# Optimization experiments

Measured on AMD Instinct MI355X. Metric: run time of the kernel, lower is better.

The kernel has to match this reference:

```python
import jax, jax.numpy as jnp
import numpy as np

ALPHA, GAMMA = 0.25, 2.0
THR = 0.85            # soft_target_threshold
KL_EPS = 1e-6
FOCAL_EPS = 1e-8
VOC = 96              # len(vocab); index VOC is blank/pad


def setup_inputs() -> dict:
    key = jax.random.key(0)
    ks = jax.random.split(key, 6)
    bs, nq, n_pts, num_gt, L = 16, 200, 25, 32, 25
    return {
        "pred_logits": jax.random.normal(ks[0], (bs, nq, n_pts, 1), jnp.float32),
        "pred_ctrl_points": jax.random.uniform(ks[1], (bs, nq, n_pts, 2), jnp.float32),
        "pred_text_logits": jax.random.normal(ks[2], (bs, nq, n_pts, VOC + 1), jnp.float32),
        "tgt_ctrl_points": jax.random.uniform(ks[3], (bs, num_gt, n_pts, 2), jnp.float32),
        "tgt_texts": jax.random.randint(ks[4], (bs, num_gt, L), 0, VOC + 1),
        "centroids": jax.random.normal(ks[5], (VOC, 256), jnp.float32),
    }


def _cost_matrix(pred_logits, pred_ctrl_points, pred_text_logits,
                 tgt_ctrl_points, tgt_texts, centroids):
    bs, nq, n_pts, _ = pred_logits.shape
    num_gt = tgt_texts.shape[1]

    # ---- focal classification cost (mean over control points) ----
    out_prob = jax.nn.sigmoid(pred_logits.reshape(bs * nq, n_pts, -1))
    neg = (1.0 - ALPHA) * out_prob ** GAMMA * (-jnp.log1p(-(out_prob - FOCAL_EPS)))
    neg = (1.0 - ALPHA) * out_prob ** GAMMA * (-jnp.log(1.0 - out_prob + FOCAL_EPS))
    pos = ALPHA * (1.0 - out_prob) ** GAMMA * (-jnp.log(out_prob + FOCAL_EPS))
    cost_class = (pos[..., 0] - neg[..., 0]).mean(-1, keepdims=True)  # [bs*nq, 1]

    # ---- L1 cdist over flattened control points ----
    out_pts = pred_ctrl_points.reshape(bs * nq, n_pts * 2)
    tgt_pts = tgt_ctrl_points.reshape(bs * num_gt, n_pts * 2)
    cost_kpts = jnp.abs(out_pts[:, None, :] - tgt_pts[None, :, :]).sum(-1)  # [bs*nq, bs*num_gt]

    # ---- linguistic KL-div cost (per-batch block diagonal) ----
    probs = jax.nn.softmax(pred_text_logits, axis=-1)          # [bs,nq,n_pts,VOC+1]
    pred_avg = probs[..., :VOC].mean(axis=2)                   # [bs,nq,VOC]
    P = pred_avg + KL_EPS
    P = P / P.sum(-1, keepdims=True)
    logP = jnp.log(P)

    # soft target distribution per character (generate_soft_target_sequence)
    cn = centroids / jnp.linalg.norm(centroids, axis=-1, keepdims=True)
    soft_all = THR * jnp.eye(VOC, dtype=P.dtype) + (1.0 - THR) * jax.nn.softmax(cn @ cn.T, axis=-1)  # [VOC,VOC]

    mask = (tgt_texts != VOC)                                  # [bs,num_gt,L]
    lengths = mask.sum(-1)                                     # [bs,num_gt]
    per_char = soft_all[jnp.clip(tgt_texts, 0, VOC - 1)]       # [bs,num_gt,L,VOC]
    tgt_avg = (per_char * mask[..., None]).sum(2) / jnp.maximum(lengths, 1)[..., None].astype(P.dtype)
    T = tgt_avg + KL_EPS
    T = T / T.sum(-1, keepdims=True)                           # [bs,num_gt,VOC]

    # KL(T || P) = sum T*logT - sum T*logP, vectorized over (query, gt)
    kl = (T * jnp.log(T)).sum(-1)[:, None, :] - jnp.einsum('bqv,bgv->bqg', logP, T)  # [bs,nq,num_gt]
    kl = jnp.where(lengths[:, None, :] == 0, 100.0, kl)

    # place per-batch blocks on the diagonal of the global cost matrix
    eye = jnp.eye(bs, dtype=kl.dtype)
    cost_text = jnp.einsum('bqg,bc->bqcg', kl, eye).reshape(bs * nq, bs * num_gt)

    C = 1.0 * cost_class + 1.0 * cost_kpts + 1.0 * cost_text   # class/coord/text weights = 1
    return C.reshape(bs, nq, bs * num_gt)


def reference(pred_logits, pred_ctrl_points, pred_text_logits,
              tgt_ctrl_points, tgt_texts, centroids):
    return _cost_matrix(pred_logits, pred_ctrl_points, pred_text_logits,
                        tgt_ctrl_points, tgt_texts, centroids)
```

## Files before the change

kernel.cpp:

```cpp
#include <hip/hip_runtime.h>
#include <hip/hip_bf16.h>

#define BS 16
#define NQ 200
#define NPTS 25
#define VOC 96
#define VOCP1 97
#define NGT 32
#define LSEQ 25
#define NCOL (BS*NGT)
#define NBQ (BS*NQ)
#define KL_EPS 1e-6f
#define FOCAL_EPS 1e-8f

__global__ __launch_bounds__(128) void kA(
        const float* __restrict__ pred_logits,
        const float* __restrict__ pred_text_logits,
        const float* __restrict__ centroids,
        float* __restrict__ logP,
        float* __restrict__ cost_class,
        float* __restrict__ soft)
{
    const int tid  = threadIdx.x;
    const int wave = tid >> 6, lane = tid & 63;
    __shared__ float s_buf[NPTS * VOCP1];
    __shared__ float s_invden[NPTS];
    __shared__ float s_part[2];

    if (blockIdx.x < NBQ) {
        const int bq = blockIdx.x;
        const float* tl = pred_text_logits + (size_t)bq * NPTS * VOCP1;
        for (int i = tid; i < NPTS * VOCP1; i += 128)
            s_buf[i] = __expf(tl[i]);
        __syncthreads();

        const int grp = tid >> 5, sub = tid & 31;
        for (int p0 = 0; p0 < NPTS; p0 += 4) {
            int p = p0 + grp;
            float s = 0.f;
            if (p < NPTS)
                for (int v = sub; v < VOCP1; v += 32) s += s_buf[p * VOCP1 + v];
            #pragma unroll
            for (int off = 16; off; off >>= 1) s += __shfl_xor(s, off, 32);
            if (p < NPTS && sub == 0) s_invden[p] = 1.0f / s;
        }

        if (wave == 0) {
            float cc = 0.f;
            if (lane < NPTS) {
                float x = pred_logits[bq * NPTS + lane];
                float p = 1.f / (1.f + __expf(-x));
                float pos = 0.25f * (1.f - p) * (1.f - p) * (-__logf(p + FOCAL_EPS));
                float neg = 0.75f * p * p * (-__logf(1.f - p + FOCAL_EPS));
                cc = pos - neg;
            }
            #pragma unroll
            for (int off = 32; off; off >>= 1) cc += __shfl_xor(cc, off);
            if (lane == 0) cost_class[bq] = cc * (1.0f / NPTS);
        }
        __syncthreads();

        float avg = 0.f;
        if (tid < VOC) {
            float a = 0.f;
            #pragma unroll
            for (int p = 0; p < NPTS; p++)
                a += s_buf[p * VOCP1 + tid] * s_invden[p];
            avg = a * (1.0f / NPTS);
        }
        float s = avg;
        #pragma unroll
        for (int off = 32; off; off >>= 1) s += __shfl_xor(s, off);
        if (lane == 0) s_part[wave] = s;
        __syncthreads();
        float denom = s_part[0] + s_part[1] + (float)VOC * KL_EPS;
        if (tid < VOC)
            logP[(size_t)bq * VOC + tid] = __logf((avg + KL_EPS) / denom);
    } else {
        const int i = blockIdx.x - NBQ;
        for (int k = tid; k < 64; k += 128)
            *(float4*)&s_buf[k * 4] = *(const float4*)&centroids[i * 256 + k * 4];
        __syncthreads();

        float e = 0.f;
        if (tid < VOC) {
            float dij = 0.f, djj = 0.f, dii = 0.f;
            const float4* cj = (const float4*)(centroids + (size_t)tid * 256);
            #pragma unroll 4
            for (int k = 0; k < 64; k++) {
                float4 b = cj[k];
                float4 a = *(const float4*)&s_buf[k * 4];
                dij += a.x * b.x + a.y * b.y + a.z * b.z + a.w * b.w;
                djj += b.x * b.x + b.y * b.y + b.z * b.z + b.w * b.w;
                dii += a.x * a.x + a.y * a.y + a.z * a.z + a.w * a.w;
            }
            float sim = dij * rsqrtf(dii * djj);
            e = __expf(sim);
        }
        float s = e;
        #pragma unroll
        for (int off = 32; off; off >>= 1) s += __shfl_xor(s, off);
        if (lane == 0) s_part[wave] = s;
        __syncthreads();
        float den = s_part[0] + s_part[1];
        if (tid < VOC) {
            float v = 0.15f * e / den;
            if (tid == i) v += 0.85f;
            soft[i * VOC + tid] = v;
        }
    }
}

__global__ __launch_bounds__(256) void kB(
        const int* __restrict__ tgt_texts,
        const float* __restrict__ soft,
        float* __restrict__ T,
        float* __restrict__ TlogT,
        int* __restrict__ lens)
{
    const int b   = blockIdx.x;
    const int tid = threadIdx.x;
    __shared__ float s_soft[VOC * VOC];
    __shared__ int   s_chars[NGT][LSEQ];

    for (int i = tid; i < VOC * VOC / 4; i += 256)
        ((float4*)s_soft)[i] = ((const float4*)soft)[i];
    for (int i = tid; i < NGT * LSEQ; i += 256)
        s_chars[i / LSEQ][i % LSEQ] = tgt_texts[b * NGT * LSEQ + i];
    __syncthreads();

    const int grp = tid >> 5, sub = tid & 31;
    for (int g = grp; g < NGT; g += 8) {
        int len = 0;
        float a0 = 0.f, a1 = 0.f, a2 = 0.f;
        for (int l = 0; l < LSEQ; l++) {
            int t = s_chars[g][l];
            if (t != VOC) {
                len++;
                const float* sr = s_soft + t * VOC;
                a0 += sr[sub]; a1 += sr[sub + 32]; a2 += sr[sub + 64];
            }
        }
        float inv = 1.f / (float)(len > 0 ? len : 1);
        a0 *= inv; a1 *= inv; a2 *= inv;
        float s = a0 + a1 + a2;
        #pragma unroll
        for (int off = 16; off; off >>= 1) s += __shfl_xor(s, off, 32);
        float denom = s + (float)VOC * KL_EPS;
        float t0 = (a0 + KL_EPS) / denom;
        float t1 = (a1 + KL_EPS) / denom;
        float t2 = (a2 + KL_EPS) / denom;
        const int bg = b * NGT + g;
        T[(size_t)bg * VOC + sub]      = t0;
        T[(size_t)bg * VOC + sub + 32] = t1;
        T[(size_t)bg * VOC + sub + 64] = t2;
        float tl = t0 * __logf(t0) + t1 * __logf(t1) + t2 * __logf(t2);
        #pragma unroll
        for (int off = 16; off; off >>= 1) tl += __shfl_xor(tl, off, 32);
        if (sub == 0) { TlogT[bg] = tl; lens[bg] = len; }
    }
}

#define TR 64
#define TC 64
__global__ __launch_bounds__(256) void kC(
        const float* __restrict__ pred_ctrl,
        const float* __restrict__ tgt_ctrl,
        const float* __restrict__ cost_class,
        float* __restrict__ out)
{
    const int r0  = (blockIdx.x >> 3) * TR;
    const int c0  = (blockIdx.x & 7) * TC;
    const int tid = threadIdx.x;
    const int tx  = tid & 15;
    const int ty  = tid >> 4;

    __shared__ float s_p[TR][52];
    __shared__ float s_t[TC][52];
    __shared__ float s_cc[TR];

    const float* pg = pred_ctrl + (size_t)r0 * 50;
    const float* tg = tgt_ctrl + (size_t)c0 * 50;
    for (int i = tid; i < TR * 50; i += 256) {
        int r = i / 50, d = i - r * 50;
        s_p[r][d] = pg[i];
        s_t[r][d] = tg[i];
    }
    if (tid < TR) s_cc[tid] = cost_class[r0 + tid];
    __syncthreads();

    float acc[4][4];
    #pragma unroll
    for (int i = 0; i < 4; i++)
        #pragma unroll
        for (int j = 0; j < 4; j++) acc[i][j] = 0.f;

    #pragma unroll
    for (int k = 0; k < 48; k += 4) {
        float4 p[4], t[4];
        #pragma unroll
        for (int i = 0; i < 4; i++) p[i] = *(const float4*)&s_p[ty * 4 + i][k];
        #pragma unroll
        for (int j = 0; j < 4; j++) t[j] = *(const float4*)&s_t[tx + 16 * j][k];
        #pragma unroll
        for (int i = 0; i < 4; i++)
            #pragma unroll
            for (int j = 0; j < 4; j++)
                acc[i][j] += fabsf(p[i].x - t[j].x) + fabsf(p[i].y - t[j].y)
                           + fabsf(p[i].z - t[j].z) + fabsf(p[i].w - t[j].w);
    }
    {
        float2 p[4], t[4];
        #pragma unroll
        for (int i = 0; i < 4; i++) p[i] = *(const float2*)&s_p[ty * 4 + i][48];
        #pragma unroll
        for (int j = 0; j < 4; j++) t[j] = *(const float2*)&s_t[tx + 16 * j][48];
        #pragma unroll
        for (int i = 0; i < 4; i++)
            #pragma unroll
            for (int j = 0; j < 4; j++)
                acc[i][j] += fabsf(p[i].x - t[j].x) + fabsf(p[i].y - t[j].y);
    }

    #pragma unroll
    for (int i = 0; i < 4; i++) {
        const int row = ty * 4 + i;
        const float cc = s_cc[row];
        #pragma unroll
        for (int j = 0; j < 4; j++)
            out[(size_t)(r0 + row) * NCOL + c0 + tx + 16 * j] = acc[i][j] + cc;
    }
}

__global__ __launch_bounds__(256) void kT(
        const float* __restrict__ logP,
        const float* __restrict__ T,
        const float* __restrict__ TlogT,
        const int* __restrict__ lens,
        float* __restrict__ out)
{
    const int r0  = blockIdx.x * 8;
    const int b   = r0 / NQ;
    const int tid = threadIdx.x;
    __shared__ float s_lp[8][VOC];
    __shared__ float s_Tt[VOC][NGT + 1];
    __shared__ float s_tl[NGT];
    __shared__ int   s_len[NGT];

    for (int i = tid; i < 8 * VOC; i += 256)
        s_lp[i / VOC][i % VOC] = logP[(size_t)r0 * VOC + i];
    for (int i = tid; i < NGT * VOC; i += 256) {
        int g = i / VOC, v = i - g * VOC;
        s_Tt[v][g] = T[(size_t)(b * NGT) * VOC + i];
    }
    if (tid < NGT) {
        s_tl[tid]  = TlogT[b * NGT + tid];
        s_len[tid] = lens[b * NGT + tid];
    }
    __syncthreads();

    const int g = tid & 31, rs = tid >> 5;
    float d = 0.f;
    #pragma unroll 8
    for (int v = 0; v < VOC; v++) d += s_lp[rs][v] * s_Tt[v][g];
    float val = (s_len[g] == 0) ? 100.f : (s_tl[g] - d);
    size_t o = (size_t)(r0 + rs) * NCOL + b * NGT + g;
    out[o] += val;
}

extern "C" void kernel_launch(void* const* d_in, const int* in_sizes, int n_in,
                              void* d_out, int out_size, void* d_ws, size_t ws_size,
                              hipStream_t stream) {
    const float* pred_logits = (const float*)d_in[0];
    const float* pred_ctrl   = (const float*)d_in[1];
    const float* pred_text   = (const float*)d_in[2];
    const float* tgt_ctrl    = (const float*)d_in[3];
    const int*   tgt_texts   = (const int*)d_in[4];
    const float* centroids   = (const float*)d_in[5];
    float* out = (float*)d_out;

    float* ws        = (float*)d_ws;
    float* logP      = ws;
    float* costclass = logP + (size_t)NBQ * VOC;
    float* soft      = costclass + NBQ;
    float* T         = soft + VOC * VOC;
    float* TlogT     = T + (size_t)NCOL * VOC;
    int*   lens      = (int*)(TlogT + NCOL);

    kA<<<NBQ + VOC, 128, 0, stream>>>(pred_logits, pred_text, centroids,
                                      logP, costclass, soft);
    kB<<<BS, 256, 0, stream>>>(tgt_texts, soft, T, TlogT, lens);
    kC<<<400, 256, 0, stream>>>(pred_ctrl, tgt_ctrl, costclass, out);
    kT<<<400, 256, 0, stream>>>(logP, T, TlogT, lens, out);
}
```

Before: 127.3 us.

## Merge four kernels into two launches, recomputing target distributions per block

New measurement: 129.0 us. About the same (+1.3%).

```diff
diff --git a/kernel.cpp b/kernel.cpp
--- a/kernel.cpp
+++ b/kernel.cpp
@@ -13,73 +13,72 @@
 #define KL_EPS 1e-6f
 #define FOCAL_EPS 1e-8f
 
-__global__ __launch_bounds__(128) void kA(
+#define NKA 1600
+#define NSOFT 96
+#define NKC 400
+
+__global__ __launch_bounds__(256) void L1(
         const float* __restrict__ pred_logits,
+        const float* __restrict__ pred_ctrl,
         const float* __restrict__ pred_text_logits,
+        const float* __restrict__ tgt_ctrl,
         const float* __restrict__ centroids,
         float* __restrict__ logP,
-        float* __restrict__ cost_class,
-        float* __restrict__ soft)
+        float* __restrict__ soft,
+        float* __restrict__ out)
 {
-    const int tid  = threadIdx.x;
-    const int wave = tid >> 6, lane = tid & 63;
-    __shared__ float s_buf[NPTS * VOCP1];
-    __shared__ float s_invden[NPTS];
-    __shared__ float s_part[2];
-
-    if (blockIdx.x < NBQ) {
-        const int bq = blockIdx.x;
+    __shared__ float smem[8320];
+    const int tid = threadIdx.x;
+
+    if (blockIdx.x < NKA) {
+        float* s_buf    = smem;
+        float* s_invden = smem + 4850;
+        float* s_part   = smem + 4900;
+        const int half = tid >> 7, htid = tid & 127;
+        const int bq   = blockIdx.x * 2 + half;
+        const int wv   = htid >> 6, lane = htid & 63;
+        float* buf = s_buf + half * (NPTS * VOCP1);
+
         const float* tl = pred_text_logits + (size_t)bq * NPTS * VOCP1;
-        for (int i = tid; i < NPTS * VOCP1; i += 128)
-            s_buf[i] = __expf(tl[i]);
-        __syncthreads();
-
-        const int grp = tid >> 5, sub = tid & 31;
+        for (int i = htid; i < NPTS * VOCP1; i += 128)
+            buf[i] = __expf(tl[i]);
+        __syncthreads();
+
+        const int grp = htid >> 5, sub = htid & 31;
         for (int p0 = 0; p0 < NPTS; p0 += 4) {
             int p = p0 + grp;
             float s = 0.f;
             if (p < NPTS)
-                for (int v = sub; v < VOCP1; v += 32) s += s_buf[p * VOCP1 + v];
+                for (int v = sub; v < VOCP1; v += 32) s += buf[p * VOCP1 + v];
             #pragma unroll
             for (int off = 16; off; off >>= 1) s += __shfl_xor(s, off, 32);
-            if (p < NPTS && sub == 0) s_invden[p] = 1.0f / s;
-        }
-
-        if (wave == 0) {
-            float cc = 0.f;
-            if (lane < NPTS) {
-                float x = pred_logits[bq * NPTS + lane];
-                float p = 1.f / (1.f + __expf(-x));
-                float pos = 0.25f * (1.f - p) * (1.f - p) * (-__logf(p + FOCAL_EPS));
-                float neg = 0.75f * p * p * (-__logf(1.f - p + FOCAL_EPS));
-                cc = pos - neg;
-            }
-            #pragma unroll
-            for (int off = 32; off; off >>= 1) cc += __shfl_xor(cc, off);
-            if (lane == 0) cost_class[bq] = cc * (1.0f / NPTS);
+            if (p < NPTS && sub == 0) s_invden[half * NPTS + p] = 1.0f / s;
         }
         __syncthreads();
 
         float avg = 0.f;
-        if (tid < VOC) {
+        if (htid < VOC) {
             float a = 0.f;
             #pragma unroll
             for (int p = 0; p < NPTS; p++)
-                a += s_buf[p * VOCP1 + tid] * s_invden[p];
+                a += buf[p * VOCP1 + htid] * s_invden[half * NPTS + p];
             avg = a * (1.0f / NPTS);
         }
         float s = avg;
         #pragma unroll
         for (int off = 32; off; off >>= 1) s += __shfl_xor(s, off);
-        if (lane == 0) s_part[wave] = s;
-        __syncthreads();
-        float denom = s_part[0] + s_part[1] + (float)VOC * KL_EPS;
-        if (tid < VOC)
-            logP[(size_t)bq * VOC + tid] = __logf((avg + KL_EPS) / denom);
-    } else {
-        const int i = blockIdx.x - NBQ;
-        for (int k = tid; k < 64; k += 128)
-            *(float4*)&s_buf[k * 4] = *(const float4*)&centroids[i * 256 + k * 4];
+        if (lane == 0) s_part[half * 2 + wv] = s;
+        __syncthreads();
+        float denom = s_part[half * 2] + s_part[half * 2 + 1] + (float)VOC * KL_EPS;
+        if (htid < VOC)
+            logP[(size_t)bq * VOC + htid] = __logf((avg + KL_EPS) / denom);
+
+    } else if (blockIdx.x < NKA + NSOFT) {
+        const int i = blockIdx.x - NKA;
+        float* s_row  = smem;
+        float* s_part = smem + 256;
+        if (tid < 64)
+            *(float4*)&s_row[tid * 4] = *(const float4*)&centroids[i * 256 + tid * 4];
         __syncthreads();
 
         float e = 0.f;
@@ -89,42 +88,124 @@
             #pragma unroll 4
             for (int k = 0; k < 64; k++) {
                 float4 b = cj[k];
-                float4 a = *(const float4*)&s_buf[k * 4];
+                float4 a = *(const float4*)&s_row[k * 4];
                 dij += a.x * b.x + a.y * b.y + a.z * b.z + a.w * b.w;
                 djj += b.x * b.x + b.y * b.y + b.z * b.z + b.w * b.w;
                 dii += a.x * a.x + a.y * a.y + a.z * a.z + a.w * a.w;
             }
-            float sim = dij * rsqrtf(dii * djj);
-            e = __expf(sim);
-        }
+            e = __expf(dij * rsqrtf(dii * djj));
+        }
+        const int wv = tid >> 6, lane = tid & 63;
         float s = e;
         #pragma unroll
         for (int off = 32; off; off >>= 1) s += __shfl_xor(s, off);
-        if (lane == 0) s_part[wave] = s;
-        __syncthreads();
-        float den = s_part[0] + s_part[1];
+        if (lane == 0) s_part[wv] = s;
+        __syncthreads();
+        float den = s_part[0] + s_part[1] + s_part[2] + s_part[3];
         if (tid < VOC) {
             float v = 0.15f * e / den;
             if (tid == i) v += 0.85f;
             soft[i * VOC + tid] = v;
         }
+    } else {
+        const int bid = blockIdx.x - (NKA + NSOFT);
+        const int r0  = (bid >> 3) * 64;
+        const int c0  = (bid & 7) * 64;
+        float* s_p  = smem;
+        float* s_t  = smem + 3328;
+        float* s_cl = smem + 6656;
+        float* s_cc = smem + 8256;
+
+        const float* pg = pred_ctrl + (size_t)r0 * 50;
+        const float* tg = tgt_ctrl + (size_t)c0 * 50;
+        for (int i = tid; i < 64 * 50; i += 256) {
+            int r = i / 50, d = i - r * 50;
+            s_p[r * 52 + d] = pg[i];
+            s_t[r * 52 + d] = tg[i];
+        }
+        for (int i = tid; i < 64 * NPTS; i += 256)
+            s_cl[i] = pred_logits[(size_t)r0 * NPTS + i];
+        __syncthreads();
+
+        if (tid < 64) {
+            float s = 0.f;
+            #pragma unroll
+            for (int l = 0; l < NPTS; l++) {
+                float x = s_cl[tid * NPTS + l];
+                float p = 1.f / (1.f + __expf(-x));
+                float pos = 0.25f * (1.f - p) * (1.f - p) * (-__logf(p + FOCAL_EPS));
+                float neg = 0.75f * p * p * (-__logf(1.f - p + FOCAL_EPS));
+                s += pos - neg;
+            }
+            s_cc[tid] = s * (1.0f / NPTS);
+        }
+        __syncthreads();
+
+        const int tx = tid & 15, ty = tid >> 4;
+        float acc[4][4];
+        #pragma unroll
+        for (int i = 0; i < 4; i++)
+            #pragma unroll
+            for (int j = 0; j < 4; j++) acc[i][j] = 0.f;
+
+        #pragma unroll
+        for (int k = 0; k < 48; k += 4) {
+            float4 p[4], t[4];
+            #pragma unroll
+            for (int i = 0; i < 4; i++) p[i] = *(const float4*)&s_p[(ty * 4 + i) * 52 + k];
+            #pragma unroll
+            for (int j = 0; j < 4; j++) t[j] = *(const float4*)&s_t[(tx + 16 * j) * 52 + k];
+            #pragma unroll
+            for (int i = 0; i < 4; i++)
+                #pragma unroll
+                for (int j = 0; j < 4; j++)
+                    acc[i][j] += fabsf(p[i].x - t[j].x) + fabsf(p[i].y - t[j].y)
+                               + fabsf(p[i].z - t[j].z) + fabsf(p[i].w - t[j].w);
+        }
+        {
+            float2 p[4], t[4];
+            #pragma unroll
+            for (int i = 0; i < 4; i++) p[i] = *(const float2*)&s_p[(ty * 4 + i) * 52 + 48];
+            #pragma unroll
+            for (int j = 0; j < 4; j++) t[j] = *(const float2*)&s_t[(tx + 16 * j) * 52 + 48];
+            #pragma unroll
+            for (int i = 0; i < 4; i++)
+                #pragma unroll
+                for (int j = 0; j < 4; j++)
+                    acc[i][j] += fabsf(p[i].x - t[j].x) + fabsf(p[i].y - t[j].y);
+        }
+
+        #pragma unroll
+        for (int i = 0; i < 4; i++) {
+            const int row = ty * 4 + i;
+            const float cc = s_cc[row];
+            #pragma unroll
+            for (int j = 0; j < 4; j++)
+                out[(size_t)(r0 + row) * NCOL + c0 + tx + 16 * j] = acc[i][j] + cc;
+        }
     }
 }
 
-__global__ __launch_bounds__(256) void kB(
+__global__ __launch_bounds__(256) void L2(
+        const float* __restrict__ logP,
+        const float* __restrict__ soft,
         const int* __restrict__ tgt_texts,
-        const float* __restrict__ soft,
-        float* __restrict__ T,
-        float* __restrict__ TlogT,
-        int* __restrict__ lens)
+        float* __restrict__ out)
 {
-    const int b   = blockIdx.x;
+    const int r0  = blockIdx.x * 8;
+    const int b   = r0 / NQ;
     const int tid = threadIdx.x;
     __shared__ float s_soft[VOC * VOC];
+    __shared__ float s_lp[8][VOC];
+    __shared__ float s_Tt[VOC][NGT + 1];
+    __shared__ float s_tl[NGT];
+    __shared__ int   s_len[NGT];
     __shared__ int   s_chars[NGT][LSEQ];
 
     for (int i = tid; i < VOC * VOC / 4; i += 256)
         ((float4*)s_soft)[i] = ((const float4*)soft)[i];
+    for (int i = tid; i < 8 * VOC; i += 256)
+        s_lp[i / VOC][i % VOC] = logP[(size_t)r0 * VOC + i];
     for (int i = tid; i < NGT * LSEQ; i += 256)
         s_chars[i / LSEQ][i % LSEQ] = tgt_texts[b * NGT * LSEQ + i];
     __syncthreads();
@@ -150,112 +231,13 @@
         float t0 = (a0 + KL_EPS) / denom;
         float t1 = (a1 + KL_EPS) / denom;
         float t2 = (a2 + KL_EPS) / denom;
-        const int bg = b * NGT + g;
-        T[(size_t)bg * VOC + sub]      = t0;
-        T[(size_t)bg * VOC + sub + 32] = t1;
-        T[(size_t)bg * VOC + sub + 64] = t2;
+        s_Tt[sub][g]      = t0;
+        s_Tt[sub + 32][g] = t1;
+        s_Tt[sub + 64][g] = t2;
         float tl = t0 * __logf(t0) + t1 * __logf(t1) + t2 * __logf(t2);
         #pragma unroll
         for (int off = 16; off; off >>= 1) tl += __shfl_xor(tl, off, 32);
-        if (sub == 0) { TlogT[bg] = tl; lens[bg] = len; }
-    }
-}
-
-#define TR 64
-#define TC 64
-__global__ __launch_bounds__(256) void kC(
-        const float* __restrict__ pred_ctrl,
-        const float* __restrict__ tgt_ctrl,
-        const float* __restrict__ cost_class,
-        float* __restrict__ out)
-{
-    const int r0  = (blockIdx.x >> 3) * TR;
-    const int c0  = (blockIdx.x & 7) * TC;
-    const int tid = threadIdx.x;
-    const int tx  = tid & 15;
-    const int ty  = tid >> 4;
-
-    __shared__ float s_p[TR][52];
-    __shared__ float s_t[TC][52];
-    __shared__ float s_cc[TR];
-
-    const float* pg = pred_ctrl + (size_t)r0 * 50;
-    const float* tg = tgt_ctrl + (size_t)c0 * 50;
-    for (int i = tid; i < TR * 50; i += 256) {
-        int r = i / 50, d = i - r * 50;
-        s_p[r][d] = pg[i];
-        s_t[r][d] = tg[i];
-    }
-    if (tid < TR) s_cc[tid] = cost_class[r0 + tid];
-    __syncthreads();
-
-    float acc[4][4];
-    #pragma unroll
-    for (int i = 0; i < 4; i++)
-        #pragma unroll
-        for (int j = 0; j < 4; j++) acc[i][j] = 0.f;
-
-    #pragma unroll
-    for (int k = 0; k < 48; k += 4) {
-        float4 p[4], t[4];
-        #pragma unroll
-        for (int i = 0; i < 4; i++) p[i] = *(const float4*)&s_p[ty * 4 + i][k];
-        #pragma unroll
-        for (int j = 0; j < 4; j++) t[j] = *(const float4*)&s_t[tx + 16 * j][k];
-        #pragma unroll
-        for (int i = 0; i < 4; i++)
-            #pragma unroll
-            for (int j = 0; j < 4; j++)
-                acc[i][j] += fabsf(p[i].x - t[j].x) + fabsf(p[i].y - t[j].y)
-                           + fabsf(p[i].z - t[j].z) + fabsf(p[i].w - t[j].w);
-    }
-    {
-        float2 p[4], t[4];
-        #pragma unroll
-        for (int i = 0; i < 4; i++) p[i] = *(const float2*)&s_p[ty * 4 + i][48];
-        #pragma unroll
-        for (int j = 0; j < 4; j++) t[j] = *(const float2*)&s_t[tx + 16 * j][48];
-        #pragma unroll
-        for (int i = 0; i < 4; i++)
-            #pragma unroll
-            for (int j = 0; j < 4; j++)
-                acc[i][j] += fabsf(p[i].x - t[j].x) + fabsf(p[i].y - t[j].y);
-    }
-
-    #pragma unroll
-    for (int i = 0; i < 4; i++) {
-        const int row = ty * 4 + i;
-        const float cc = s_cc[row];
-        #pragma unroll
-        for (int j = 0; j < 4; j++)
-            out[(size_t)(r0 + row) * NCOL + c0 + tx + 16 * j] = acc[i][j] + cc;
-    }
-}
-
-__global__ __launch_bounds__(256) void kT(
-        const float* __restrict__ logP,
-        const float* __restrict__ T,
-        const float* __restrict__ TlogT,
-        const int* __restrict__ lens,
-        float* __restrict__ out)
-{
-    const int r0  = blockIdx.x * 8;
-    const int b   = r0 / NQ;
-    const int tid = threadIdx.x;
-    __shared__ float s_lp[8][VOC];
-    __shared__ float s_Tt[VOC][NGT + 1];
-    __shared__ float s_tl[NGT];
-    __shared__ int   s_len[NGT];
-
-    for (int i = tid; i < 8 * VOC; i += 256)
-        s_lp[i / VOC][i % VOC] = logP[(size_t)r0 * VOC + i];
-    for (int i = tid; i < NGT * VOC; i += 256) {
-        int g = i / VOC, v = i - g * VOC;
-        s_Tt[v][g] = T[(size_t)(b * NGT) * VOC + i];
-    }
-    if (tid < NGT) {
-        s_tl[tid]  = TlogT[b * NGT + tid];
-        s_len[tid] = lens[b * NGT + tid];
+        if (sub == 0) { s_tl[g] = tl; s_len[g] = len; }
     }
     __syncthreads();
 
@@ -264,8 +246,7 @@
     #pragma unroll 8
     for (int v = 0; v < VOC; v++) d += s_lp[rs][v] * s_Tt[v][g];
     float val = (s_len[g] == 0) ? 100.f : (s_tl[g] - d);
-    size_t o = (size_t)(r0 + rs) * NCOL + b * NGT + g;
-    out[o] += val;
+    out[(size_t)(r0 + rs) * NCOL + b * NGT + g] += val;
 }
 
 extern "C" void kernel_launch(void* const* d_in, const int* in_sizes, int n_in,
@@ -279,17 +260,12 @@
     const float* centroids   = (const float*)d_in[5];
     float* out = (float*)d_out;
 
-    float* ws        = (float*)d_ws;
-    float* logP      = ws;
-    float* costclass = logP + (size_t)NBQ * VOC;
-    float* soft      = costclass + NBQ;
-    float* T         = soft + VOC * VOC;
-    float* TlogT     = T + (size_t)NCOL * VOC;
-    int*   lens      = (int*)(TlogT + NCOL);
-
-    kA<<<NBQ + VOC, 128, 0, stream>>>(pred_logits, pred_text, centroids,
-                                      logP, costclass, soft);
-    kB<<<BS, 256, 0, stream>>>(tgt_texts, soft, T, TlogT, lens);
-    kC<<<400, 256, 0, stream>>>(pred_ctrl, tgt_ctrl, costclass, out);
-    kT<<<400, 256, 0, stream>>>(logP, T, TlogT, lens, out);
+    float* ws   = (float*)d_ws;
+    float* logP = ws;
+    float* soft = logP + (size_t)NBQ * VOC;
+
+    L1<<<NKA + NSOFT + NKC, 256, 0, stream>>>(
+        pred_logits, pred_ctrl, pred_text, tgt_ctrl, centroids,
+        logP, soft, out);
+    L2<<<NKC, 256, 0, stream>>>(logP, soft, tgt_texts, out);
 }
```
